# Kernel optimization log

Hardware: AMD Instinct MI355X
Metric: run time of the kernel (lower is better)

The kernel has to match this reference:

```python
import jax, jax.numpy as jnp
import numpy as np

NUM_HEADS = 8
MASK_NEG = -1e30


def setup_inputs() -> dict:
    key = jax.random.key(0)
    k1, k2, k3 = jax.random.split(key, 3)
    B, S, D = 8, 2048, 128
    queries = jax.random.normal(k1, (B, S, D), dtype=jnp.float32)
    mask = jnp.ones((B, S), dtype=jnp.float32)
    # kernel_size=1 Conv1D with no bias == dense matmul over last dim
    W_q = jax.random.normal(k2, (D, D), dtype=jnp.float32) * (D ** -0.5)
    W_mem = jax.random.normal(k3, (D, 2 * D), dtype=jnp.float32) * (D ** -0.5)
    return {"queries": queries, "mask": mask, "W_q": W_q, "W_mem": W_mem}


def _split_heads(x, h):
    # [B, S, D] -> [B, h, S, D/h]
    B, S, D = x.shape
    return x.reshape(B, S, h, D // h).transpose(0, 2, 1, 3)


def reference(queries, mask, W_q, W_mem):
    B, S, D = queries.shape
    h = NUM_HEADS
    scale = (D // h) ** -0.5
    memory = jnp.einsum('bsd,de->bse', queries, W_mem)   # [B,S,2D]
    query = jnp.einsum('bsd,de->bse', queries, W_q)      # [B,S,D]
    K, V = jnp.split(memory, 2, axis=2)
    Q = _split_heads(query, h) * scale                   # [B,h,S,dh]
    K = _split_heads(K, h)
    V = _split_heads(V, h)
    logits = jnp.einsum('bhqd,bhkd->bhqk', Q, K)         # [B,h,S,S]
    m = mask.reshape(B, 1, 1, S)
    logits = logits + (1.0 - m) * MASK_NEG
    weights = jax.nn.softmax(logits, axis=-1)
    # dropout is identity at inference (training=None)
    x = jnp.einsum('bhqk,bhkd->bhqd', weights, V)        # [B,h,S,dh]
    return x.transpose(0, 2, 1, 3).reshape(B, S, D)
```

## Files before the change

kernel.cpp:

```cpp
#include <hip/hip_runtime.h>
#include <hip/hip_bf16.h>
#include <stdint.h>

#define B_    8
#define S_    2048
#define D_    128
#define H_    8
#define DH_   16
#define BH_   64
#define E_    384
#define NT_   (S_ / 32)

typedef __attribute__((ext_vector_type(4)))  short short4v;
typedef __attribute__((ext_vector_type(8)))  short short8;
typedef __attribute__((ext_vector_type(4)))  float f32x4;
typedef __attribute__((ext_vector_type(16))) float f32x16;

__device__ inline unsigned short f2b(float f) {
    union { __bf16 h; unsigned short u; } t;
    t.h = (__bf16)f;
    return t.u;
}
__device__ inline float b2f(unsigned short u) {
    union { unsigned u; float f; } x; x.u = ((unsigned)u) << 16; return x.f;
}
__device__ inline int dperm(int d) {
    return (d & 3) | ((d & 8) >> 1) | ((d & 4) << 1);
}

__device__ inline void gload_lds16(const void* g, void* l) {
    __builtin_amdgcn_global_load_lds(
        (const __attribute__((address_space(1))) unsigned int*)g,
        (__attribute__((address_space(3))) unsigned int*)l, 16, 0, 0);
}

#define EXPB 16250.7346f

__global__ void wtrans_kernel(const float* __restrict__ Wq,
                              const float* __restrict__ Wmem,
                              unsigned short* __restrict__ wt) {
    int e = blockIdx.x, k = threadIdx.x;
    float v = (e < 128) ? Wq[k * 128 + e] : Wmem[k * 256 + (e - 128)];
    wt[e * 128 + k] = f2b(v);
}

__global__ __launch_bounds__(512) void proj_kernel(
        const float* __restrict__ X, const float* __restrict__ mask,
        const unsigned short* __restrict__ wt,
        unsigned short* __restrict__ Qb, unsigned short* __restrict__ KVf) {
    __shared__ unsigned short Xs[64][136];
    __shared__ unsigned short Vs[64][136];
    __shared__ __align__(16) unsigned short Qls[64][136];
    __shared__ __align__(16) unsigned short Kls[8][2][64][8];
    __shared__ float Ms[64];
    const int tid = threadIdx.x;
    const int b = blockIdx.x & 7, st = blockIdx.x >> 3;
    const int s0 = st * 64;
    const float* Xp = X + ((size_t)b * S_ + s0) * D_;

    for (int i = tid; i < 64 * D_ / 4; i += 512) {
        f32x4 v = __builtin_nontemporal_load((const f32x4*)Xp + i);
        int row = i >> 5, c4 = (i & 31) * 4;
        Xs[row][c4 + 0] = f2b(v[0]); Xs[row][c4 + 1] = f2b(v[1]);
        Xs[row][c4 + 2] = f2b(v[2]); Xs[row][c4 + 3] = f2b(v[3]);
    }
    if (tid < 64) Ms[tid] = mask[(size_t)b * S_ + s0 + tid];
    __syncthreads();

    const int wid = tid >> 6, lane = tid & 63;
    const int lr = lane & 15, lg = lane >> 4;
    const float qscale = 0.25f * 1.44269504088896f;

    for (int ci = 0; ci < 3; ++ci) {
        const int ct = wid + ci * 8;
        const int e0 = ct * 16;
        short4v bfr[8];
        #pragma unroll
        for (int kk = 0; kk < 8; ++kk)
            bfr[kk] = *(const short4v*)&wt[(e0 + lr) * 128 + kk * 16 + lg * 4];
        for (int rt = 0; rt < 4; ++rt) {
            f32x4 acc; acc[0] = acc[1] = acc[2] = acc[3] = 0.f;
            #pragma unroll
            for (int kk = 0; kk < 8; ++kk) {
                short4v a = *(const short4v*)&Xs[rt * 16 + lr][kk * 16 + lg * 4];
                acc = __builtin_amdgcn_mfma_f32_16x16x16bf16_1k(a, bfr[kk], acc, 0, 0, 0);
            }
            const int e = e0 + lr;
            #pragma unroll
            for (int r = 0; r < 4; ++r) {
                const int sl = rt * 16 + lg * 4 + r;
                const float v = acc[r];
                if (e < 128) {
                    int hh = e >> 4, d = dperm(e & 15);
                    Qls[sl][hh * 16 + d] = f2b(v * qscale);
                } else if (e < 256) {
                    int ek = e - 128, hh = ek >> 4, d = dperm(ek & 15);
                    int t = sl >> 5, qq = sl & 31;
                    int l = qq + 32 * (d >> 3), jj = d & 7;
                    Kls[hh][t][l][jj] = f2b(v);
                } else {
                    Vs[sl][e - 256] = f2b(v);
                }
            }
        }
    }
    __syncthreads();

    for (int c = tid; c < 1024; c += 512) {
        const int hh = c >> 7, sl = (c >> 1) & 63, half = c & 1;
        *(short8*)&Qb[(((size_t)b * H_ + hh) * S_ + s0 + sl) * DH_ + half * 8] =
            *(const short8*)&Qls[sl][hh * 16 + half * 8];
    }
    for (int c = tid; c < 1024; c += 512) {
        const int hh = c >> 7, t = (c >> 6) & 1, lc = c & 63;
        *(short8*)&KVf[((size_t)(b * H_ + hh) * NT_ + st * 2 + t) * 1536 + lc * 8] =
            *(const short8*)&Kls[hh][t][lc][0];
    }

    for (int j = tid; j < H_ * 2 * 2 * 64; j += 512) {
        const int l = j & 63, f = (j >> 6) & 1, t = (j >> 7) & 1, hh = j >> 8;
        const int q = l & 31, h = l >> 5;
        const int vrow = (q < 16) ? q : 16;
        const int T = st * 2 + t;
        unsigned short* dst =
            KVf + ((size_t)(b * H_ + hh) * NT_ + T) * 1536 + (1 + f) * 512 + l * 8;
        union { unsigned short us[8]; short8 v; } o;
        #pragma unroll
        for (int e = 0; e < 8; ++e) {
            const int p = f * 16 + 8 * h + e;
            const int sl = (p & 16) | dperm(p & 15);
            const int srow = t * 32 + sl;
            const float mk = Ms[srow];
            o.us[e] = f2b((vrow == 16) ? mk : b2f(Vs[srow][hh * 16 + vrow]) * mk);
        }
        *(short8*)dst = o.v;
    }
}

__global__ __launch_bounds__(512, 4) void attn_kernel(
        const unsigned short* __restrict__ Qb, const unsigned short* __restrict__ KVf,
        float* __restrict__ out) {
    const int tid = threadIdx.x;
    const int wid = tid >> 6, lane = tid & 63;
    const int q = lane & 31, h = lane >> 5;
    const int p = blockIdx.x;
    const int bh = (p & 7) * 8 + ((p >> 3) & 7);
    const int qs = p >> 6;
    const int q0 = qs * 256 + wid * 32;

    __shared__ unsigned short buf[2][8][3][64][8];

    const unsigned short* kv = KVf + (size_t)bh * NT_ * 1536 + (size_t)lane * 8;

    const short8 qf = *(const short8*)&Qb[((size_t)bh * S_ + q0 + q) * DH_ + 8 * h];

    f32x16 accA, accB, z;
    #pragma unroll
    for (int i = 0; i < 16; ++i) { accA[i] = 0.f; accB[i] = 0.f; z[i] = 0.f; }

    f32x16 sA, sB;
    short8 pA0, pA1, pB0, pB1;

#define STAGE(C_)                                                              \
    {                                                                          \
        const int tt_ = (C_) * 4 + (wid & 3) + ((wid >> 2) * 32);              \
        const unsigned short* g_ = kv + (size_t)tt_ * 1536;                    \
        unsigned short* d_ = &buf[(C_) & 1][wid][0][0][0];                     \
        gload_lds16(g_,        d_);                                            \
        gload_lds16(g_ + 512,  d_ + 512);                                      \
        gload_lds16(g_ + 1024, d_ + 1024);                                     \
    }

#define FENCE_BAR()                                                            \
    asm volatile("s_waitcnt lgkmcnt(0) vmcnt(0)" ::: "memory");                \
    __builtin_amdgcn_sched_barrier(0);                                         \
    __builtin_amdgcn_s_barrier();                                              \
    __builtin_amdgcn_sched_barrier(0);

#define EXP_PV(ACC_, S_, V0_, V1_)                                             \
    {                                                                          \
        union { unsigned u[4]; short8 v; } b0, b1;                             \
        _Pragma("unroll")                                                      \
        for (int i = 0; i < 4; ++i) {                                          \
            const int l0 = (int)__builtin_fmaf(S_[2 * i],     128.f, EXPB);    \
            const int h0 = (int)__builtin_fmaf(S_[2 * i + 1], 128.f, EXPB);    \
            b0.u[i] = (unsigned)l0 | ((unsigned)h0 << 16);                     \
            const int l1 = (int)__builtin_fmaf(S_[8 + 2 * i],     128.f, EXPB);\
            const int h1 = (int)__builtin_fmaf(S_[8 + 2 * i + 1], 128.f, EXPB);\
            b1.u[i] = (unsigned)l1 | ((unsigned)h1 << 16);                     \
        }                                                                      \
        ACC_ = __builtin_amdgcn_mfma_f32_32x32x16_bf16(V0_, b0.v, ACC_, 0, 0, 0); \
        ACC_ = __builtin_amdgcn_mfma_f32_32x32x16_bf16(V1_, b1.v, ACC_, 0, 0, 0); \
    }

#define PAIR_STEP(BI_, I_)                                                     \
    {                                                                          \
        const short8 kfA = *(const short8*)&buf[BI_][I_][0][lane][0];          \
        const short8 nA0 = *(const short8*)&buf[BI_][I_][1][lane][0];          \
        const short8 nA1 = *(const short8*)&buf[BI_][I_][2][lane][0];          \
        const short8 kfB = *(const short8*)&buf[BI_][4 + I_][0][lane][0];      \
        const short8 nB0 = *(const short8*)&buf[BI_][4 + I_][1][lane][0];      \
        const short8 nB1 = *(const short8*)&buf[BI_][4 + I_][2][lane][0];      \
        f32x16 nsA = __builtin_amdgcn_mfma_f32_32x32x16_bf16(kfA, qf, z, 0, 0, 0); \
        f32x16 nsB = __builtin_amdgcn_mfma_f32_32x32x16_bf16(kfB, qf, z, 0, 0, 0); \
        EXP_PV(accA, sA, pA0, pA1);                                            \
        EXP_PV(accB, sB, pB0, pB1);                                            \
        sA = nsA; sB = nsB;                                                    \
        pA0 = nA0; pA1 = nA1; pB0 = nB0; pB1 = nB1;                            \
    }

#define PRIME(BI_, I_)                                                         \
    {                                                                          \
        const short8 kfA = *(const short8*)&buf[BI_][I_][0][lane][0];          \
        pA0 = *(const short8*)&buf[BI_][I_][1][lane][0];                       \
        pA1 = *(const short8*)&buf[BI_][I_][2][lane][0];                       \
        const short8 kfB = *(const short8*)&buf[BI_][4 + I_][0][lane][0];      \
        pB0 = *(const short8*)&buf[BI_][4 + I_][1][lane][0];                   \
        pB1 = *(const short8*)&buf[BI_][4 + I_][2][lane][0];                   \
        sA = __builtin_amdgcn_mfma_f32_32x32x16_bf16(kfA, qf, z, 0, 0, 0);     \
        sB = __builtin_amdgcn_mfma_f32_32x32x16_bf16(kfB, qf, z, 0, 0, 0);     \
    }

    STAGE(0);
    FENCE_BAR();
    STAGE(1);
    PRIME(0, 0);

    for (int c = 0; c < 8; ++c) {
        if (c > 0) {
            FENCE_BAR();
            if (c < 7) STAGE(c + 1);
        }
        #pragma unroll
        for (int i = 0; i < 4; ++i) {
            if (c == 0 && i == 0) continue;
            PAIR_STEP(c & 1, i);
        }
    }
    EXP_PV(accA, sA, pA0, pA1);
    EXP_PV(accB, sB, pB0, pB1);
#undef STAGE
#undef FENCE_BAR
#undef EXP_PV
#undef PAIR_STEP
#undef PRIME

    const int b = bh >> 3, head = bh & 7;
    float* obase = out + ((size_t)b * S_ + q0 + q) * D_ + head * DH_ + 4 * h;
    float o[16];
    #pragma unroll
    for (int i = 0; i < 16; ++i) o[i] = accA[i] + accB[i];
    const float r = 1.0f / o[8];
    *(float4*)obase       = make_float4(o[0] * r, o[1] * r, o[2] * r, o[3] * r);
    *(float4*)(obase + 8) = make_float4(o[4] * r, o[5] * r, o[6] * r, o[7] * r);
}

extern "C" void kernel_launch(void* const* d_in, const int* in_sizes, int n_in,
                              void* d_out, int out_size, void* d_ws, size_t ws_size,
                              hipStream_t stream) {
    const float* X    = (const float*)d_in[0];
    const float* mask = (const float*)d_in[1];
    const float* Wq   = (const float*)d_in[2];
    const float* Wmem = (const float*)d_in[3];
    float* out = (float*)d_out;

    unsigned short* Qb  = (unsigned short*)d_ws;
    unsigned short* KVf = Qb + (size_t)BH_ * S_ * DH_;
    unsigned short* wt  = KVf + (size_t)BH_ * NT_ * 1536;

    wtrans_kernel<<<E_, 128, 0, stream>>>(Wq, Wmem, wt);
    proj_kernel<<<B_ * S_ / 64, 512, 0, stream>>>(X, mask, wt, Qb, KVf);
    attn_kernel<<<BH_ * 8, 512, 0, stream>>>(Qb, KVf, out);
}
```

Before: 54.58 us.

## Split projection kernel into Q, K, V block types to triple grid size

The projection kernel now launches three times as many blocks, each computing only one of Q, K or V for a 64-row tile, and shares one LDS buffer. The aim is more parallelism and lower LDS use per block, which allows higher occupancy across the GPU's compute units. The cost is that each block type re-reads and re-converts the same X tile, tripling X global reads.

```diff
diff --git a/kernel.cpp b/kernel.cpp
--- a/kernel.cpp
+++ b/kernel.cpp
@@ -49,12 +49,12 @@
         const unsigned short* __restrict__ wt,
         unsigned short* __restrict__ Qb, unsigned short* __restrict__ KVf) {
     __shared__ unsigned short Xs[64][136];
-    __shared__ unsigned short Vs[64][136];
-    __shared__ __align__(16) unsigned short Qls[64][136];
-    __shared__ __align__(16) unsigned short Kls[8][2][64][8];
+    __shared__ __align__(16) unsigned short Wk[64][136];
     __shared__ float Ms[64];
     const int tid = threadIdx.x;
-    const int b = blockIdx.x & 7, st = blockIdx.x >> 3;
+    const int typ = blockIdx.x >> 8;
+    const int r   = blockIdx.x & 255;
+    const int b = r & 7, st = r >> 3;
     const int s0 = st * 64;
     const float* Xp = X + ((size_t)b * S_ + s0) * D_;
 
@@ -64,15 +64,17 @@
         Xs[row][c4 + 0] = f2b(v[0]); Xs[row][c4 + 1] = f2b(v[1]);
         Xs[row][c4 + 2] = f2b(v[2]); Xs[row][c4 + 3] = f2b(v[3]);
     }
-    if (tid < 64) Ms[tid] = mask[(size_t)b * S_ + s0 + tid];
+    if (typ == 2 && tid < 64) Ms[tid] = mask[(size_t)b * S_ + s0 + tid];
     __syncthreads();
 
     const int wid = tid >> 6, lane = tid & 63;
     const int lr = lane & 15, lg = lane >> 4;
     const float qscale = 0.25f * 1.44269504088896f;
 
-    for (int ci = 0; ci < 3; ++ci) {
-        const int ct = wid + ci * 8;
+    unsigned short (*Kls)[2][64][8] = (unsigned short (*)[2][64][8]) & Wk[0][0];
+
+    {
+        const int ct = wid + typ * 8;
         const int e0 = ct * 16;
         short4v bfr[8];
         #pragma unroll
@@ -87,53 +89,56 @@
             }
             const int e = e0 + lr;
             #pragma unroll
-            for (int r = 0; r < 4; ++r) {
-                const int sl = rt * 16 + lg * 4 + r;
-                const float v = acc[r];
-                if (e < 128) {
+            for (int r2 = 0; r2 < 4; ++r2) {
+                const int sl = rt * 16 + lg * 4 + r2;
+                const float v = acc[r2];
+                if (typ == 0) {
                     int hh = e >> 4, d = dperm(e & 15);
-                    Qls[sl][hh * 16 + d] = f2b(v * qscale);
-                } else if (e < 256) {
+                    Wk[sl][hh * 16 + d] = f2b(v * qscale);
+                } else if (typ == 1) {
                     int ek = e - 128, hh = ek >> 4, d = dperm(ek & 15);
                     int t = sl >> 5, qq = sl & 31;
                     int l = qq + 32 * (d >> 3), jj = d & 7;
                     Kls[hh][t][l][jj] = f2b(v);
                 } else {
-                    Vs[sl][e - 256] = f2b(v);
+                    Wk[sl][e - 256] = f2b(v);
                 }
             }
         }
     }
     __syncthreads();
 
-    for (int c = tid; c < 1024; c += 512) {
-        const int hh = c >> 7, sl = (c >> 1) & 63, half = c & 1;
-        *(short8*)&Qb[(((size_t)b * H_ + hh) * S_ + s0 + sl) * DH_ + half * 8] =
-            *(const short8*)&Qls[sl][hh * 16 + half * 8];
-    }
-    for (int c = tid; c < 1024; c += 512) {
-        const int hh = c >> 7, t = (c >> 6) & 1, lc = c & 63;
-        *(short8*)&KVf[((size_t)(b * H_ + hh) * NT_ + st * 2 + t) * 1536 + lc * 8] =
-            *(const short8*)&Kls[hh][t][lc][0];
-    }
-
-    for (int j = tid; j < H_ * 2 * 2 * 64; j += 512) {
-        const int l = j & 63, f = (j >> 6) & 1, t = (j >> 7) & 1, hh = j >> 8;
-        const int q = l & 31, h = l >> 5;
-        const int vrow = (q < 16) ? q : 16;
-        const int T = st * 2 + t;
-        unsigned short* dst =
-            KVf + ((size_t)(b * H_ + hh) * NT_ + T) * 1536 + (1 + f) * 512 + l * 8;
-        union { unsigned short us[8]; short8 v; } o;
-        #pragma unroll
-        for (int e = 0; e < 8; ++e) {
-            const int p = f * 16 + 8 * h + e;
-            const int sl = (p & 16) | dperm(p & 15);
-            const int srow = t * 32 + sl;
-            const float mk = Ms[srow];
-            o.us[e] = f2b((vrow == 16) ? mk : b2f(Vs[srow][hh * 16 + vrow]) * mk);
-        }
-        *(short8*)dst = o.v;
+    if (typ == 0) {
+        for (int c = tid; c < 1024; c += 512) {
+            const int hh = c >> 7, sl = (c >> 1) & 63, half = c & 1;
+            *(short8*)&Qb[(((size_t)b * H_ + hh) * S_ + s0 + sl) * DH_ + half * 8] =
+                *(const short8*)&Wk[sl][hh * 16 + half * 8];
+        }
+    } else if (typ == 1) {
+        for (int c = tid; c < 1024; c += 512) {
+            const int hh = c >> 7, t = (c >> 6) & 1, lc = c & 63;
+            *(short8*)&KVf[((size_t)(b * H_ + hh) * NT_ + st * 2 + t) * 1536 + lc * 8] =
+                *(const short8*)&Kls[hh][t][lc][0];
+        }
+    } else {
+        for (int j = tid; j < H_ * 2 * 2 * 64; j += 512) {
+            const int l = j & 63, f = (j >> 6) & 1, t = (j >> 7) & 1, hh = j >> 8;
+            const int q = l & 31, h = l >> 5;
+            const int vrow = (q < 16) ? q : 16;
+            const int T = st * 2 + t;
+            unsigned short* dst =
+                KVf + ((size_t)(b * H_ + hh) * NT_ + T) * 1536 + (1 + f) * 512 + l * 8;
+            union { unsigned short us[8]; short8 v; } o;
+            #pragma unroll
+            for (int e = 0; e < 8; ++e) {
+                const int p = f * 16 + 8 * h + e;
+                const int sl = (p & 16) | dperm(p & 15);
+                const int srow = t * 32 + sl;
+                const float mk = Ms[srow];
+                o.us[e] = f2b((vrow == 16) ? mk : b2f(Wk[srow][hh * 16 + vrow]) * mk);
+            }
+            *(short8*)dst = o.v;
+        }
     }
 }
 
@@ -269,6 +274,6 @@
     unsigned short* wt  = KVf + (size_t)BH_ * NT_ * 1536;
 
     wtrans_kernel<<<E_, 128, 0, stream>>>(Wq, Wmem, wt);
-    proj_kernel<<<B_ * S_ / 64, 512, 0, stream>>>(X, mask, wt, Qb, KVf);
+    proj_kernel<<<3 * (B_ * S_ / 64), 512, 0, stream>>>(X, mask, wt, Qb, KVf);
     attn_kernel<<<BH_ * 8, 512, 0, stream>>>(Qb, KVf, out);
 }
```

Measured after the change: 55.70 us. 1.02x slower.
